# Kernel optimization log

Measured on AMD Instinct MI355X. Metric: run time of the kernel, lower is better.

The kernel has to match this reference:

```python
import jax, jax.numpy as jnp
import numpy as np

B, C, L = 8, 1024, 1024
H = 16
D = C // H  # 64 samples per head
GROUPS = 32  # GroupNorm32: channels > 64 -> 32 groups
EPS = 1e-5


def setup_inputs() -> dict:
    key = jax.random.key(0)
    ks = jax.random.split(key, 5)
    x = jax.random.normal(ks[0], (B, C, L), dtype=jnp.float32)
    gn_weight = jnp.ones((C,), jnp.float32)
    gn_bias = jnp.zeros((C,), jnp.float32)
    qkv_w = jax.random.normal(ks[1], (3 * C, C), jnp.float32) * 0.02
    qkv_b = jax.random.normal(ks[2], (3 * C,), jnp.float32) * 0.02
    out_w = jax.random.normal(ks[3], (C, C), jnp.float32) * 0.02
    out_b = jax.random.normal(ks[4], (C,), jnp.float32) * 0.02
    return {"x": x, "gn_weight": gn_weight, "gn_bias": gn_bias,
            "qkv_w": qkv_w, "qkv_b": qkv_b, "out_w": out_w, "out_b": out_b,
            "qk_bias": 0}


def _group_norm(x, w, b):
    # x: [B, C, L]; normalize over (C//GROUPS, L) per group, in float32
    xg = x.astype(jnp.float32).reshape(B, GROUPS, -1)
    mu = xg.mean(axis=-1, keepdims=True)
    var = xg.var(axis=-1, keepdims=True)
    xn = ((xg - mu) * jax.lax.rsqrt(var + EPS)).reshape(B, C, L)
    return (xn * w[None, :, None] + b[None, :, None]).astype(x.dtype)


def reference(x, gn_weight, gn_bias, qkv_w, qkv_b, out_w, out_b, qk_bias):
    scale = 1.0 / np.sqrt(D).astype(np.float32)
    xn = _group_norm(x, gn_weight, gn_bias)
    # 1x1 conv == pointwise matmul over channels
    qkv = jnp.einsum('oc,bcl->bol', qkv_w, xn) + qkv_b[None, :, None]  # [B,3C,L]
    # reshape (B, H, 3D, L) and split exactly as torch .split(D, dim=2)
    qkv = qkv.reshape(B, H, 3 * D, L)
    q, k, v = qkv[:, :, :D], qkv[:, :, D:2 * D], qkv[:, :, 2 * D:]
    q = jnp.swapaxes(q, -1, -2) * scale  # [B,H,L,D]
    k = k * scale                        # [B,H,D,L]
    v = jnp.swapaxes(v, -1, -2)          # [B,H,L,D]
    score = jnp.einsum('bhld,bhdm->bhlm', q, k) + qk_bias  # [B,H,L,L]
    weights = jax.nn.softmax(score.astype(jnp.float32), axis=-1)
    ctx = jnp.einsum('bhlm,bhmd->bhld', weights, v)  # [B,H,L,D]
    ctx = jnp.swapaxes(ctx, -1, -2).reshape(B, C, L)
    h = jnp.einsum('oc,bcl->bol', out_w, ctx) + out_b[None, :, None]
    return xn + h  # residual uses the normalized x, as in the source
```

## Files before the change

### kernel.cpp

```cpp
#include <hip/hip_runtime.h>

using bf16x8 = __attribute__((ext_vector_type(8))) __bf16;
using f32x4  = __attribute__((ext_vector_type(4))) float;

#define DEV __device__ __forceinline__

DEV unsigned short f2bf(float f){
  unsigned u = __builtin_bit_cast(unsigned, f);
  u += 0x7fffu + ((u >> 16) & 1u);
  return (unsigned short)(u >> 16);
}

DEV void load_lds16(const void* g, void* l){
  __builtin_amdgcn_global_load_lds((const __attribute__((address_space(1))) unsigned*)g,
                                   (__attribute__((address_space(3))) unsigned*)l, 16, 0, 0);
}

DEV f32x4 mfma16(bf16x8 a, bf16x8 b, f32x4 c){
  return __builtin_amdgcn_mfma_f32_16x16x32_bf16(a, b, c, 0, 0, 0);
}

__global__ void wconv_k(const float* __restrict__ a, unsigned short* __restrict__ o, int n4){
  for (int i = blockIdx.x * blockDim.x + threadIdx.x; i < n4; i += gridDim.x * blockDim.x){
    float4 v = reinterpret_cast<const float4*>(a)[i];
    ushort4 u;
    u.x = f2bf(v.x); u.y = f2bf(v.y); u.z = f2bf(v.z); u.w = f2bf(v.w);
    reinterpret_cast<ushort4*>(o)[i] = u;
  }
}

__global__ __launch_bounds__(256) void gn_stats_k(const float* __restrict__ x, float* __restrict__ st){
  int bg = blockIdx.x;
  const float4* xp = reinterpret_cast<const float4*>(x + (size_t)bg * 32768);
  float s = 0.f, ss = 0.f;
  for (int i = threadIdx.x; i < 8192; i += 256){
    float4 v = xp[i];
    s  += (v.x + v.y) + (v.z + v.w);
    ss += (v.x*v.x + v.y*v.y) + (v.z*v.z + v.w*v.w);
  }
  #pragma unroll
  for (int off = 32; off; off >>= 1){ s += __shfl_down(s, off); ss += __shfl_down(ss, off); }
  __shared__ float rs[4], rss[4];
  if ((threadIdx.x & 63) == 0){ rs[threadIdx.x >> 6] = s; rss[threadIdx.x >> 6] = ss; }
  __syncthreads();
  if (threadIdx.x == 0){
    s  = (rs[0] + rs[1]) + (rs[2] + rs[3]);
    ss = (rss[0] + rss[1]) + (rss[2] + rss[3]);
    float mu  = s * (1.0f / 32768.0f);
    float var = ss * (1.0f / 32768.0f) - mu * mu;
    st[bg*2]   = mu;
    st[bg*2+1] = rsqrtf(var + 1e-5f);
  }
}

__global__ __launch_bounds__(256) void gn_norm_k(const float* __restrict__ x,
                                                 const float* __restrict__ gw,
                                                 const float* __restrict__ gb,
                                                 const float* __restrict__ st,
                                                 float* __restrict__ xn,
                                                 unsigned short* __restrict__ xnt){
  int t = blockIdx.x;
  int tile = t & 15; int g = (t >> 4) & 31; int bb = t >> 9;
  float mu = st[(bb*32+g)*2], rstd = st[(bb*32+g)*2+1];
  __shared__ unsigned short lt[64*32];
  int tid = threadIdx.x;
  int l = tid & 63;
  int c0 = tid >> 6;
  size_t base = ((size_t)bb*1024 + g*32) * 1024 + tile*64;
  #pragma unroll
  for (int cb = 0; cb < 8; ++cb){
    int c = cb*4 + c0;
    size_t idx = base + (size_t)c*1024 + l;
    float xv = x[idx];
    int cg = g*32 + c;
    float v = (xv - mu) * rstd * gw[cg] + gb[cg];
    xn[idx] = v;
    lt[l*32 + c] = f2bf(v);
  }
  __syncthreads();
  int lr = tid >> 2, sl = tid & 3;
  uint4 u = *reinterpret_cast<uint4*>(&lt[lr*32 + sl*8]);
  size_t ob = ((size_t)bb*1024 + tile*64 + lr) * 1024 + g*32 + sl*8;
  *reinterpret_cast<uint4*>(&xnt[ob]) = u;
}

template<int MODE>
__global__ __launch_bounds__(256) void gemm_k(const unsigned short* __restrict__ A,
                                              const unsigned short* __restrict__ Bm,
                                              const float* __restrict__ bias,
                                              float* __restrict__ outf,
                                              unsigned short* __restrict__ qo,
                                              unsigned short* __restrict__ ko,
                                              unsigned short* __restrict__ vo){
  constexpr int MT = MODE ? 8 : 24;
  __shared__ char sA[16384];
  __shared__ char sB[16384];
  const int tid = threadIdx.x;
  const int w = tid >> 6, ln = tid & 63, hi = ln >> 4, lo = ln & 15;
  const int wrow = w >> 1, wcol = w & 1;
  const int bx = blockIdx.x;
  const int b = bx / (MT*8);
  const int rem = bx % (MT*8);
  const int mt = rem >> 3, nt = rem & 7;
  const char* Ag = (const char*)A + (size_t)mt*128*2048;
  const char* Bg = (const char*)Bm + ((size_t)b*1024 + nt*128)*2048;
  f32x4 acc[4][4] = {};
  for (int kk = 0; kk < 16; ++kk){
    #pragma unroll
    for (int i = 0; i < 4; ++i){
      int s = tid*16 + i*4096;
      int row = s >> 7;
      int byte = (s & 127) ^ ((row & 7) << 4);
      size_t off = (size_t)row*2048 + kk*128 + byte;
      load_lds16(Ag + off, sA + s);
      load_lds16(Bg + off, sB + s);
    }
    __syncthreads();
    #pragma unroll
    for (int ks = 0; ks < 2; ++ks){
      bf16x8 af[4], bq[4];
      #pragma unroll
      for (int mi = 0; mi < 4; ++mi){
        int row = wrow*64 + mi*16 + lo;
        af[mi] = *reinterpret_cast<const bf16x8*>(sA + row*128 + ((ks*64 + hi*16) ^ ((row & 7) << 4)));
      }
      #pragma unroll
      for (int ni = 0; ni < 4; ++ni){
        int row = wcol*64 + ni*16 + lo;
        bq[ni] = *reinterpret_cast<const bf16x8*>(sB + row*128 + ((ks*64 + hi*16) ^ ((row & 7) << 4)));
      }
      #pragma unroll
      for (int mi = 0; mi < 4; ++mi)
        #pragma unroll
        for (int ni = 0; ni < 4; ++ni)
          acc[mi][ni] = mfma16(af[mi], bq[ni], acc[mi][ni]);
    }
    __syncthreads();
  }
  if (MODE == 0){
    #pragma unroll
    for (int mi = 0; mi < 4; ++mi){
      const int o0 = mt*128 + wrow*64 + mi*16 + hi*4;
      const int hh = o0 / 192;
      const int rr = o0 % 192;
      const size_t hb = (size_t)b*16 + hh;
      float bv0 = bias[o0], bv1 = bias[o0+1], bv2 = bias[o0+2], bv3 = bias[o0+3];
      #pragma unroll
      for (int ni = 0; ni < 4; ++ni){
        const int l = nt*128 + wcol*64 + ni*16 + lo;
        if (rr < 64){
          ushort4 u;
          u.x = f2bf(acc[mi][ni][0] + bv0); u.y = f2bf(acc[mi][ni][1] + bv1);
          u.z = f2bf(acc[mi][ni][2] + bv2); u.w = f2bf(acc[mi][ni][3] + bv3);
          *reinterpret_cast<ushort4*>(qo + (hb*1024 + l)*64 + rr) = u;
        } else if (rr < 128){
          ushort4 u;
          u.x = f2bf(acc[mi][ni][0] + bv0); u.y = f2bf(acc[mi][ni][1] + bv1);
          u.z = f2bf(acc[mi][ni][2] + bv2); u.w = f2bf(acc[mi][ni][3] + bv3);
          *reinterpret_cast<ushort4*>(ko + (hb*1024 + l)*64 + (rr - 64)) = u;
        } else {
          const int d = rr - 128;
          vo[(hb*64 + d + 0)*1024 + l] = f2bf(acc[mi][ni][0] + bv0);
          vo[(hb*64 + d + 1)*1024 + l] = f2bf(acc[mi][ni][1] + bv1);
          vo[(hb*64 + d + 2)*1024 + l] = f2bf(acc[mi][ni][2] + bv2);
          vo[(hb*64 + d + 3)*1024 + l] = f2bf(acc[mi][ni][3] + bv3);
        }
      }
    }
  } else {
    #pragma unroll
    for (int mi = 0; mi < 4; ++mi){
      const int o0 = mt*128 + wrow*64 + mi*16 + hi*4;
      #pragma unroll
      for (int ni = 0; ni < 4; ++ni){
        const int l = nt*128 + wcol*64 + ni*16 + lo;
        #pragma unroll
        for (int r = 0; r < 4; ++r){
          size_t idx = ((size_t)b*1024 + o0 + r) * 1024 + l;
          outf[idx] += acc[mi][ni][r] + bias[o0 + r];
        }
      }
    }
  }
}

__global__ __launch_bounds__(256) void attn_k(const unsigned short* __restrict__ qt,
                                              const unsigned short* __restrict__ kt,
                                              const unsigned short* __restrict__ vt,
                                              unsigned short* __restrict__ ctx){
  __shared__ char sK[8192];
  __shared__ char sV[8192];
  __shared__ char sP[8192];
  const int tid = threadIdx.x;
  const int w = tid >> 6, ln = tid & 63, hi = ln >> 4, lo = ln & 15;
  const int bx = blockIdx.x;
  const int qb = bx & 15;
  const int bh = bx >> 4;
  const int qrow = qb*64 + w*16 + lo;
  const unsigned short* qp = qt + ((size_t)bh*1024 + qrow) * 64;
  bf16x8 qf0 = *reinterpret_cast<const bf16x8*>(qp + hi*8);
  bf16x8 qf1 = *reinterpret_cast<const bf16x8*>(qp + 32 + hi*8);
  const char* kg = (const char*)(kt + (size_t)bh*65536);
  const char* vg = (const char*)(vt + (size_t)bh*65536);
  f32x4 oa[4] = {};
  float mrow[4] = {-1e30f, -1e30f, -1e30f, -1e30f};
  float lrow[4] = {0.f, 0.f, 0.f, 0.f};
  char* pw = sP + w*2048;
  for (int kb = 0; kb < 16; ++kb){
    #pragma unroll
    for (int i = 0; i < 2; ++i){
      int s = tid*16 + i*4096;
      int row = s >> 7;
      int byte = (s & 127) ^ ((row & 7) << 4);
      load_lds16(kg + (size_t)(kb*64 + row)*128 + byte, sK + s);
      load_lds16(vg + (size_t)row*2048 + kb*128 + byte, sV + s);
    }
    __syncthreads();
    f32x4 sf[4];
    #pragma unroll
    for (int nf = 0; nf < 4; ++nf){
      int kr = nf*16 + lo;
      const char* kbase = sK + kr*128;
      int sw = (kr & 7) << 4;
      bf16x8 k0 = *reinterpret_cast<const bf16x8*>(kbase + ((hi*16) ^ sw));
      bf16x8 k1 = *reinterpret_cast<const bf16x8*>(kbase + ((64 + hi*16) ^ sw));
      f32x4 t = {};
      t = mfma16(qf0, k0, t);
      t = mfma16(qf1, k1, t);
      sf[nf] = t * 0.015625f;
    }
    float corr[4];
    #pragma unroll
    for (int r = 0; r < 4; ++r){
      float mx = fmaxf(fmaxf(sf[0][r], sf[1][r]), fmaxf(sf[2][r], sf[3][r]));
      #pragma unroll
      for (int off = 1; off < 16; off <<= 1) mx = fmaxf(mx, __shfl_xor(mx, off));
      float mn = fmaxf(mrow[r], mx);
      corr[r] = __expf(mrow[r] - mn);
      mrow[r] = mn;
      float ps = 0.f;
      #pragma unroll
      for (int nf = 0; nf < 4; ++nf){
        float p = __expf(sf[nf][r] - mn);
        sf[nf][r] = p;
        ps += p;
      }
      #pragma unroll
      for (int off = 1; off < 16; off <<= 1) ps += __shfl_xor(ps, off);
      lrow[r] = lrow[r]*corr[r] + ps;
    }
    #pragma unroll
    for (int df = 0; df < 4; ++df){
      oa[df][0] *= corr[0]; oa[df][1] *= corr[1];
      oa[df][2] *= corr[2]; oa[df][3] *= corr[3];
    }
    #pragma unroll
    for (int nf = 0; nf < 4; ++nf){
      #pragma unroll
      for (int r = 0; r < 4; ++r){
        int pr = hi*4 + r;
        int colb = (nf*16 + lo) * 2;
        *reinterpret_cast<unsigned short*>(pw + pr*128 + (colb ^ ((pr & 7) << 4))) = f2bf(sf[nf][r]);
      }
    }
    #pragma unroll
    for (int half = 0; half < 2; ++half){
      bf16x8 pa = *reinterpret_cast<const bf16x8*>(pw + lo*128 + ((half*64 + hi*16) ^ ((lo & 7) << 4)));
      #pragma unroll
      for (int df = 0; df < 4; ++df){
        int vr = df*16 + lo;
        bf16x8 vf = *reinterpret_cast<const bf16x8*>(sV + vr*128 + ((half*64 + hi*16) ^ ((vr & 7) << 4)));
        oa[df] = mfma16(pa, vf, oa[df]);
      }
    }
    __syncthreads();
  }
  const int b = bh >> 4, h = bh & 15;
  #pragma unroll
  for (int df = 0; df < 4; ++df){
    #pragma unroll
    for (int r = 0; r < 4; ++r){
      int l = qb*64 + w*16 + hi*4 + r;
      int c = h*64 + df*16 + lo;
      ctx[((size_t)b*1024 + l)*1024 + c] = f2bf(oa[df][r] / lrow[r]);
    }
  }
}

extern "C" void kernel_launch(void* const* d_in, const int* in_sizes, int n_in,
                              void* d_out, int out_size, void* d_ws, size_t ws_size,
                              hipStream_t stream) {
  (void)in_sizes; (void)n_in; (void)out_size; (void)ws_size;
  const float* x     = (const float*)d_in[0];
  const float* gn_w  = (const float*)d_in[1];
  const float* gn_b  = (const float*)d_in[2];
  const float* qkv_w = (const float*)d_in[3];
  const float* qkv_b = (const float*)d_in[4];
  const float* out_w = (const float*)d_in[5];
  const float* out_b = (const float*)d_in[6];
  float* out = (float*)d_out;
  char* ws = (char*)d_ws;
  unsigned short* xnt  = (unsigned short*)(ws);
  unsigned short* qwb  = (unsigned short*)(ws + 16777216);
  unsigned short* owb  = (unsigned short*)(ws + 23068672);
  unsigned short* qt   = (unsigned short*)(ws + 25165824);
  unsigned short* kt   = (unsigned short*)(ws + 41943040);
  unsigned short* vs   = (unsigned short*)(ws + 58720256);
  unsigned short* ctxt = (unsigned short*)(ws + 75497472);
  float*          st   = (float*)(ws + 92274688);

  wconv_k<<<512, 256, 0, stream>>>(qkv_w, qwb, 786432);
  wconv_k<<<512, 256, 0, stream>>>(out_w, owb, 262144);
  gn_stats_k<<<256, 256, 0, stream>>>(x, st);
  gn_norm_k<<<4096, 256, 0, stream>>>(x, gn_w, gn_b, st, out, xnt);
  gemm_k<0><<<1536, 256, 0, stream>>>(qwb, xnt, qkv_b, nullptr, qt, kt, vs);
  attn_k<<<2048, 256, 0, stream>>>(qt, kt, vs, ctxt);
  gemm_k<1><<<512, 256, 0, stream>>>(owb, ctxt, out_b, out, nullptr, nullptr, nullptr);
}
```

Before: 343.0 us.

## Double-buffer attention K/V tiles, lazy softmax rescale, transposed P reads, XCD remap

The attention kernel now double-buffers K/V in LDS, prefetching the next tile while the current one is computed, and keeps one barrier per iteration. Softmax moves to exp2 with the scale folded in, and rescaling is skipped unless the running max grows by more than a threshold. P is packed with v_cvt_pk_bf16 and read back with ds_read_b64_tr_b16 transposed loads, and the final divide becomes a reciprocal multiply. Both the GEMM and attention kernels remap block indices across the 8 XCDs for better L2 locality. The changes add inline asm and hand-placed waitcnts, which carry some risk of ordering or correctness mistakes.

```diff
diff --git a/kernel.cpp b/kernel.cpp
--- a/kernel.cpp
+++ b/kernel.cpp
@@ -2,6 +2,8 @@
 
 using bf16x8 = __attribute__((ext_vector_type(8))) __bf16;
 using f32x4  = __attribute__((ext_vector_type(4))) float;
+typedef __attribute__((ext_vector_type(2))) unsigned u32x2;
+typedef __attribute__((ext_vector_type(4))) unsigned u32x4;
 
 #define DEV __device__ __forceinline__
 
@@ -18,6 +20,27 @@
 
 DEV f32x4 mfma16(bf16x8 a, bf16x8 b, f32x4 c){
   return __builtin_amdgcn_mfma_f32_16x16x32_bf16(a, b, c, 0, 0, 0);
+}
+
+DEV float exp2_hw(float x){
+  float r;
+  asm("v_exp_f32 %0, %1" : "=v"(r) : "v"(x));
+  return r;
+}
+
+DEV unsigned cvtpk_bf16(float a, float b){
+  unsigned r;
+  asm("v_cvt_pk_bf16_f32 %0, %1, %2" : "=v"(r) : "v"(a), "v"(b));
+  return r;
+}
+
+DEV u32x2 tr_read(const void* p){
+  u32x2 r;
+  asm volatile("ds_read_b64_tr_b16 %0, %1"
+               : "=v"(r)
+               : "v"((const __attribute__((address_space(3))) char*)p)
+               : "memory");
+  return r;
 }
 
 __global__ void wconv_k(const float* __restrict__ a, unsigned short* __restrict__ o, int n4){
@@ -93,12 +116,14 @@
                                               unsigned short* __restrict__ ko,
                                               unsigned short* __restrict__ vo){
   constexpr int MT = MODE ? 8 : 24;
+  constexpr int CHUNK = MT * 8;
   __shared__ char sA[16384];
   __shared__ char sB[16384];
   const int tid = threadIdx.x;
   const int w = tid >> 6, ln = tid & 63, hi = ln >> 4, lo = ln & 15;
   const int wrow = w >> 1, wcol = w & 1;
-  const int bx = blockIdx.x;
+  const int bxo = (int)blockIdx.x;
+  const int bx = (bxo & 7) * CHUNK + (bxo >> 3);
   const int b = bx / (MT*8);
   const int rem = bx % (MT*8);
   const int mt = rem >> 3, nt = rem & 7;
@@ -188,12 +213,13 @@
                                               const unsigned short* __restrict__ kt,
                                               const unsigned short* __restrict__ vt,
                                               unsigned short* __restrict__ ctx){
-  __shared__ char sK[8192];
-  __shared__ char sV[8192];
+  __shared__ char sK[2][8192];
+  __shared__ char sV[2][8192];
   __shared__ char sP[8192];
   const int tid = threadIdx.x;
   const int w = tid >> 6, ln = tid & 63, hi = ln >> 4, lo = ln & 15;
-  const int bx = blockIdx.x;
+  const int bxo = (int)blockIdx.x;
+  const int bx = (bxo & 7) * 256 + (bxo >> 3);
   const int qb = bx & 15;
   const int bh = bx >> 4;
   const int qrow = qb*64 + w*16 + lo;
@@ -206,83 +232,123 @@
   float mrow[4] = {-1e30f, -1e30f, -1e30f, -1e30f};
   float lrow[4] = {0.f, 0.f, 0.f, 0.f};
   char* pw = sP + w*2048;
-  for (int kb = 0; kb < 16; ++kb){
+
+  auto STAGE = [&](int buf, int kb){
     #pragma unroll
     for (int i = 0; i < 2; ++i){
       int s = tid*16 + i*4096;
       int row = s >> 7;
       int byte = (s & 127) ^ ((row & 7) << 4);
-      load_lds16(kg + (size_t)(kb*64 + row)*128 + byte, sK + s);
-      load_lds16(vg + (size_t)row*2048 + kb*128 + byte, sV + s);
-    }
-    __syncthreads();
+      load_lds16(kg + (size_t)(kb*64 + row)*128 + byte, sK[buf] + s);
+      load_lds16(vg + (size_t)row*2048 + kb*128 + byte, sV[buf] + s);
+    }
+  };
+
+  const float sc2 = 0.015625f * 1.44269504f;
+
+  STAGE(0, 0);
+  asm volatile("s_waitcnt vmcnt(0)" ::: "memory");
+  __builtin_amdgcn_s_barrier();
+
+  for (int kb = 0; kb < 16; ++kb){
+    const int cur = kb & 1;
+    STAGE(cur ^ 1, (kb + 1) & 15);
+
     f32x4 sf[4];
     #pragma unroll
     for (int nf = 0; nf < 4; ++nf){
       int kr = nf*16 + lo;
-      const char* kbase = sK + kr*128;
+      const char* kbase = sK[cur] + kr*128;
       int sw = (kr & 7) << 4;
       bf16x8 k0 = *reinterpret_cast<const bf16x8*>(kbase + ((hi*16) ^ sw));
       bf16x8 k1 = *reinterpret_cast<const bf16x8*>(kbase + ((64 + hi*16) ^ sw));
       f32x4 t = {};
       t = mfma16(qf0, k0, t);
       t = mfma16(qf1, k1, t);
-      sf[nf] = t * 0.015625f;
-    }
-    float corr[4];
+      sf[nf] = t;
+    }
+
+    float m2b[4];
     #pragma unroll
     for (int r = 0; r < 4; ++r){
-      float mx = fmaxf(fmaxf(sf[0][r], sf[1][r]), fmaxf(sf[2][r], sf[3][r]));
-      #pragma unroll
-      for (int off = 1; off < 16; off <<= 1) mx = fmaxf(mx, __shfl_xor(mx, off));
-      float mn = fmaxf(mrow[r], mx);
-      corr[r] = __expf(mrow[r] - mn);
-      mrow[r] = mn;
-      float ps = 0.f;
-      #pragma unroll
-      for (int nf = 0; nf < 4; ++nf){
-        float p = __expf(sf[nf][r] - mn);
-        sf[nf][r] = p;
-        ps += p;
-      }
+      float bm = fmaxf(fmaxf(sf[0][r], sf[1][r]), fmaxf(sf[2][r], sf[3][r]));
+      #pragma unroll
+      for (int off = 1; off < 16; off <<= 1) bm = fmaxf(bm, __shfl_xor(bm, off));
+      m2b[r] = bm * sc2;
+    }
+
+    int need = (m2b[0] > mrow[0] + 8.f) | (m2b[1] > mrow[1] + 8.f) |
+               (m2b[2] > mrow[2] + 8.f) | (m2b[3] > mrow[3] + 8.f);
+    if (__any(need)){
+      #pragma unroll
+      for (int r = 0; r < 4; ++r){
+        float nm = fmaxf(mrow[r], m2b[r]);
+        float corr = exp2_hw(mrow[r] - nm);
+        mrow[r] = nm;
+        lrow[r] *= corr;
+        oa[0][r] *= corr; oa[1][r] *= corr; oa[2][r] *= corr; oa[3][r] *= corr;
+      }
+    }
+
+    f32x4 psum = {};
+    #pragma unroll
+    for (int nf = 0; nf < 4; ++nf){
+      float p0 = exp2_hw(fmaf(sf[nf][0], sc2, -mrow[0]));
+      float p1 = exp2_hw(fmaf(sf[nf][1], sc2, -mrow[1]));
+      float p2 = exp2_hw(fmaf(sf[nf][2], sc2, -mrow[2]));
+      float p3 = exp2_hw(fmaf(sf[nf][3], sc2, -mrow[3]));
+      psum[0] += p0; psum[1] += p1; psum[2] += p2; psum[3] += p3;
+      u32x2 pk;
+      pk.x = cvtpk_bf16(p0, p1);
+      pk.y = cvtpk_bf16(p2, p3);
+      *reinterpret_cast<u32x2*>(pw + (nf*16 + lo)*32 + hi*8) = pk;
+    }
+    #pragma unroll
+    for (int r = 0; r < 4; ++r){
+      float ps = psum[r];
       #pragma unroll
       for (int off = 1; off < 16; off <<= 1) ps += __shfl_xor(ps, off);
-      lrow[r] = lrow[r]*corr[r] + ps;
-    }
+      lrow[r] += ps;
+    }
+
+    asm volatile("s_waitcnt lgkmcnt(0)" ::: "memory");
+    const char* pb = pw + lo*2 + hi*256;
+    u32x2 t00 = tr_read(pb);
+    u32x2 t01 = tr_read(pb + 128);
+    u32x2 t10 = tr_read(pb + 1024);
+    u32x2 t11 = tr_read(pb + 1024 + 128);
+    asm volatile("s_waitcnt lgkmcnt(0)" ::: "memory");
+    __builtin_amdgcn_sched_barrier(0);
+    u32x4 pc0; pc0.x = t00.x; pc0.y = t00.y; pc0.z = t01.x; pc0.w = t01.y;
+    u32x4 pc1; pc1.x = t10.x; pc1.y = t10.y; pc1.z = t11.x; pc1.w = t11.y;
+    bf16x8 pa0 = __builtin_bit_cast(bf16x8, pc0);
+    bf16x8 pa1 = __builtin_bit_cast(bf16x8, pc1);
     #pragma unroll
     for (int df = 0; df < 4; ++df){
-      oa[df][0] *= corr[0]; oa[df][1] *= corr[1];
-      oa[df][2] *= corr[2]; oa[df][3] *= corr[3];
-    }
-    #pragma unroll
-    for (int nf = 0; nf < 4; ++nf){
-      #pragma unroll
-      for (int r = 0; r < 4; ++r){
-        int pr = hi*4 + r;
-        int colb = (nf*16 + lo) * 2;
-        *reinterpret_cast<unsigned short*>(pw + pr*128 + (colb ^ ((pr & 7) << 4))) = f2bf(sf[nf][r]);
-      }
-    }
-    #pragma unroll
-    for (int half = 0; half < 2; ++half){
-      bf16x8 pa = *reinterpret_cast<const bf16x8*>(pw + lo*128 + ((half*64 + hi*16) ^ ((lo & 7) << 4)));
-      #pragma unroll
-      for (int df = 0; df < 4; ++df){
-        int vr = df*16 + lo;
-        bf16x8 vf = *reinterpret_cast<const bf16x8*>(sV + vr*128 + ((half*64 + hi*16) ^ ((vr & 7) << 4)));
-        oa[df] = mfma16(pa, vf, oa[df]);
-      }
-    }
-    __syncthreads();
-  }
+      int vr = df*16 + lo;
+      const char* vb = sV[cur] + vr*128;
+      int sw = (vr & 7) << 4;
+      bf16x8 v0 = *reinterpret_cast<const bf16x8*>(vb + ((hi*16) ^ sw));
+      bf16x8 v1 = *reinterpret_cast<const bf16x8*>(vb + ((64 + hi*16) ^ sw));
+      oa[df] = mfma16(pa0, v0, oa[df]);
+      oa[df] = mfma16(pa1, v1, oa[df]);
+    }
+
+    asm volatile("s_waitcnt vmcnt(0)" ::: "memory");
+    __builtin_amdgcn_s_barrier();
+  }
+
   const int b = bh >> 4, h = bh & 15;
+  float inv[4];
+  #pragma unroll
+  for (int r = 0; r < 4; ++r) inv[r] = __builtin_amdgcn_rcpf(lrow[r]);
   #pragma unroll
   for (int df = 0; df < 4; ++df){
     #pragma unroll
     for (int r = 0; r < 4; ++r){
       int l = qb*64 + w*16 + hi*4 + r;
       int c = h*64 + df*16 + lo;
-      ctx[((size_t)b*1024 + l)*1024 + c] = f2bf(oa[df][r] / lrow[r]);
+      ctx[((size_t)b*1024 + l)*1024 + c] = f2bf(oa[df][r] * inv[r]);
     }
   }
 }
```

Measured after the change: 335.1 us. 2.3% less time.
